# Performance work log

Hardware: AMD Instinct MI355X
Metric: run time of the kernel (lower is better)

Reference implementation:

```python
import jax, jax.numpy as jnp
import numpy as np

N = 100000   # nodes
E = 1600000  # edges (before self-loops)
H = 4        # heads
C = 16       # out channels per head
NEG_SLOPE = 0.2


def _gat_layer(x, src, dst, W, a_src, a_dst, b):
    # x: [N, Fin]; W: [Fin, H*C]; a_src/a_dst: [H, C]; b: [H*C]
    h = (x @ W).reshape(N, H, C)                       # [N, H, C]
    e_s = jnp.einsum('nhc,hc->nh', h, a_src)           # [N, H]
    e_d = jnp.einsum('nhc,hc->nh', h, a_dst)           # [N, H]
    e = e_s[src] + e_d[dst]                            # [E', H]
    e = jax.nn.leaky_relu(e, NEG_SLOPE)
    # segment softmax over destination nodes
    m = jax.ops.segment_max(e, dst, num_segments=N)    # [N, H]
    ex = jnp.exp(e - m[dst])
    s = jax.ops.segment_sum(ex, dst, num_segments=N)   # [N, H]
    alpha = ex / (s[dst] + 1e-16)                      # [E', H]
    msg = alpha[:, :, None] * h[src]                   # [E', H, C]
    out = jax.ops.segment_sum(msg, dst, num_segments=N)  # [N, H, C]
    return out.reshape(N, H * C) + b


def setup_inputs() -> dict:
    key = jax.random.key(0)
    ks = jax.random.split(key, 24)
    g = lambda k, shp, sc=0.1: (jax.random.normal(k, shp, jnp.float32) * sc)
    inp = {
        'x': jax.random.normal(ks[0], (N, 1), jnp.float32),
        'edge_index': jax.random.randint(ks[1], (2, E), 0, N, dtype=jnp.int32),
        # GAT layer 0: in=1
        'W0': g(ks[2], (1, H * C)), 'as0': g(ks[3], (H, C)), 'ad0': g(ks[4], (H, C)), 'b0': jnp.zeros((H * C,), jnp.float32),
        # GAT layer 1: in=64
        'W1': g(ks[5], (H * C, H * C)), 'as1': g(ks[6], (H, C)), 'ad1': g(ks[7], (H, C)), 'b1': jnp.zeros((H * C,), jnp.float32),
        # GAT layer 2: in=64
        'W2': g(ks[8], (H * C, H * C)), 'as2': g(ks[9], (H, C)), 'ad2': g(ks[10], (H, C)), 'b2': jnp.zeros((H * C,), jnp.float32),
        # latent MLP: Linear(64,64) -> ReLU -> Linear(64,16)
        'lw1': g(ks[11], (H * C, 64)), 'lb1': jnp.zeros((64,), jnp.float32),
        'lw2': g(ks[12], (64, 16)), 'lb2': jnp.zeros((16,), jnp.float32),
        # decoder: Linear(16,4) -> Softmax
        'dw': g(ks[13], (16, 4)), 'db': jnp.zeros((4,), jnp.float32),
    }
    return inp


def reference(x, edge_index, W0, as0, ad0, b0, W1, as1, ad1, b1, W2, as2, ad2, b2, lw1, lb1, lw2, lb2, dw, db):
    # add self-loops (PyG GATConv default add_self_loops=True)
    loops = jnp.arange(N, dtype=edge_index.dtype)
    src = jnp.concatenate([edge_index[0], loops])
    dst = jnp.concatenate([edge_index[1], loops])
    h = _gat_layer(x, src, dst, W0, as0, ad0, b0)
    h = _gat_layer(h, src, dst, W1, as1, ad1, b1)
    h = _gat_layer(h, src, dst, W2, as2, ad2, b2)
    h = jax.nn.relu(h @ lw1 + lb1)
    h = h @ lw2 + lb2
    logits = h @ dw + db
    return jax.nn.softmax(logits, axis=-1)
```

## Files before the change

kernel.cpp:

```cpp
#include <hip/hip_runtime.h>
#include <hip/hip_fp16.h>
#include <math.h>

#define NN 100000
#define EE 1600000
#define EP (EE + NN)
#define NEG 0.2f
#define TN 128
#define BW 256
#define NB 391
#define CHUNK 4096
#define SSTRIDE 5120
#define SCAP 5120

typedef __attribute__((ext_vector_type(2))) float floatx2;

__device__ inline unsigned pk_fp8x4(float a, float b, float c, float d) {
    unsigned r = __builtin_amdgcn_cvt_pk_fp8_f32(a, b, 0u, false);
    r = __builtin_amdgcn_cvt_pk_fp8_f32(c, d, r, true);
    return r;
}

__device__ __forceinline__ void accum_fp8p(uint2 raw, float p, floatx2* acc) {
    floatx2 p2; p2[0] = p; p2[1] = p;
    acc[0] += p2 * __builtin_amdgcn_cvt_pk_f32_fp8(raw.x, false);
    acc[1] += p2 * __builtin_amdgcn_cvt_pk_f32_fp8(raw.x, true);
    acc[2] += p2 * __builtin_amdgcn_cvt_pk_f32_fp8(raw.y, false);
    acc[3] += p2 * __builtin_amdgcn_cvt_pk_f32_fp8(raw.y, true);
}

__device__ __forceinline__ int wave_iscan(int v, int lane) {
#pragma unroll
    for (int o = 1; o < 64; o <<= 1) {
        int t = __shfl_up(v, o);
        if (lane >= o) v += t;
    }
    return v;
}


__global__ __launch_bounds__(512) void partition_k(const int* __restrict__ ei, int* __restrict__ gcur,
                                                   unsigned int* __restrict__ arena) {
    __shared__ int lh[512], lcur[512], lbase[512];
    __shared__ int wsum[8];
    __shared__ unsigned int staged[CHUNK];
    __shared__ unsigned short stb[CHUNK];
    int tid = threadIdx.x;
    int lane = tid & 63, wid = tid >> 6;
    int c0 = blockIdx.x * CHUNK;
    int csize = min(CHUNK, EP - c0);
    lh[tid] = 0;
    __syncthreads();
    unsigned int myv[8];
    int myb[8];
#pragma unroll
    for (int i = 0; i < 8; i++) {
        int e = c0 + i * 512 + tid;
        if (e < c0 + csize) {
            int d = (e < EE) ? ei[EE + e] : (e - EE);
            int sv = (e < EE) ? ei[e] : d;
            int b = d >> 8;
            myv[i] = ((unsigned)(d - (b << 8)) << 17) | (unsigned)sv;
            myb[i] = b;
            atomicAdd(&lh[b], 1);
        } else myb[i] = -1;
    }
    __syncthreads();
    int v = lh[tid];
    int isc = wave_iscan(v, lane);
    if (lane == 63) wsum[wid] = isc;
    __syncthreads();
    if (tid == 0) {
        int run = 0;
#pragma unroll
        for (int w = 0; w < 8; w++) { int t = wsum[w]; wsum[w] = run; run += t; }
    }
    __syncthreads();
    int excl = isc - v + wsum[wid];
    lcur[tid] = excl;
    __syncthreads();
#pragma unroll
    for (int i = 0; i < 8; i++) {
        if (myb[i] >= 0) {
            int idx = atomicAdd(&lcur[myb[i]], 1);
            staged[idx] = myv[i];
            stb[idx] = (unsigned short)myb[i];
        }
    }
    __syncthreads();
    if (tid < NB && v > 0) {
        int base = atomicAdd(&gcur[tid], v);
        lbase[tid] = tid * SSTRIDE + base - excl;
    }
    __syncthreads();
    for (int i = tid; i < csize; i += 512) {
        unsigned int val = staged[i];
        arena[lbase[stb[i]] + i] = val;
    }
}

__global__ __launch_bounds__(512) void bscan_k(const int* __restrict__ gcur, int* __restrict__ bbase,
                                               int* __restrict__ rowptr) {
    __shared__ int s[512];
    int tid = threadIdx.x;
    int v = (tid < NB) ? gcur[tid] : 0;
    s[tid] = v;
    __syncthreads();
    for (int o = 1; o < 512; o <<= 1) {
        int t = (tid >= o) ? s[tid - o] : 0;
        __syncthreads();
        s[tid] += t;
        __syncthreads();
    }
    int excl = s[tid] - v;
    if (tid <= NB) bbase[tid] = excl;
    if (tid == 0) rowptr[NN] = EP;
}

__global__ __launch_bounds__(512) void csr_scatter_k(const int* __restrict__ bbase, const int* __restrict__ gcur,
                                                     const unsigned int* __restrict__ arena,
                                                     int* __restrict__ rowptr, int* __restrict__ edge_src) {
    __shared__ int cnt[256], sc[256];
    __shared__ int wsum[4];
    __shared__ unsigned int stg[SCAP];
    int tid = threadIdx.x;
    int b = blockIdx.x;
    int e0 = bbase[b];
    int sz = gcur[b];
    int abase = b * SSTRIDE;
    if (tid < 256) cnt[tid] = 0;
    __syncthreads();
    for (int i = tid; i < sz; i += 512) {
        unsigned int v = arena[abase + i];
        if (i < SCAP) stg[i] = v;
        atomicAdd(&cnt[v >> 17], 1);
    }
    __syncthreads();
    if (tid < 256) {
        int lane = tid & 63, wid = tid >> 6;
        int v = cnt[tid];
        int isc = wave_iscan(v, lane);
        if (lane == 63) wsum[wid] = isc;
        __syncthreads();
        if (tid == 0) {
            int run = 0;
#pragma unroll
            for (int w = 0; w < 4; w++) { int t = wsum[w]; wsum[w] = run; run += t; }
        }
        __syncthreads();
        int excl = isc - v + wsum[wid];
        int d = (b << 8) + tid;
        if (d < NN) rowptr[d] = e0 + excl;
        sc[tid] = excl;
    } else {
        __syncthreads();
        __syncthreads();
    }
    __syncthreads();
    for (int i = tid; i < sz; i += 512) {
        unsigned int val = (i < SCAP) ? stg[i] : arena[abase + i];
        int dl = val >> 17;
        int p = atomicAdd(&sc[dl], 1);
        edge_src[e0 + p] = (int)(val & 0x1FFFFu);
    }
}


__global__ __launch_bounds__(256) void gather0_k(const float* __restrict__ x, const float* __restrict__ W0,
                                                 const float* __restrict__ as_, const float* __restrict__ ad_,
                                                 const int* __restrict__ rowptr, const int* __restrict__ edge_src,
                                                 const float* __restrict__ b, __half* __restrict__ hout) {
    __shared__ float W0l[64], asl[64], adl[64], bl[64];
    int tid = threadIdx.x;
    if (tid < 64) { W0l[tid] = W0[tid]; asl[tid] = as_[tid]; adl[tid] = ad_[tid]; bl[tid] = b[tid]; }
    __syncthreads();
    int wv = (blockIdx.x * 256 + tid) >> 6;
    int lane = tid & 63;
    if (wv >= NN) return;
    int q = lane >> 2, head = lane & 3;
    float cs = 0.f, cd = 0.f;
#pragma unroll
    for (int c = 0; c < 16; c++) {
        float w = W0l[head * 16 + c];
        cs += w * asl[head * 16 + c];
        cd += w * adl[head * 16 + c];
    }
    int beg = rowptr[wv], end = rowptr[wv + 1];
    float xd = x[wv];
    float num = 0.f, den = 0.f;
    for (int e0 = beg; e0 < end; e0 += 16) {
        int e = e0 + q;
        bool vld = e < end;
        int ee = vld ? e : (end - 1);
        int src = edge_src[ee];
        float xs = x[src];
        float ev = xs * cs + xd * cd;
        ev = ev > 0.f ? ev : NEG * ev;
        float p = vld ? __expf(ev) : 0.f;
        num += p * xs;
        den += p;
    }
    num += __shfl_xor(num, 4);  num += __shfl_xor(num, 8);
    num += __shfl_xor(num, 16); num += __shfl_xor(num, 32);
    den += __shfl_xor(den, 4);  den += __shfl_xor(den, 8);
    den += __shfl_xor(den, 16); den += __shfl_xor(den, 32);
    float nh = __shfl(num, lane >> 4);
    float dh = __shfl(den, lane >> 4);
    float val = nh / (dh + 1e-16f);
    float hv = val * W0l[lane] + bl[lane];
    hout[((size_t)wv << 6) + lane] = __float2half(hv);
}


__global__ __launch_bounds__(256) void transform64_k(const __half* __restrict__ hin, const float* __restrict__ W,
                                                     const float* __restrict__ as_, const float* __restrict__ ad_,
                                                     unsigned char* __restrict__ h8, float* __restrict__ es, float* __restrict__ ed) {
    __shared__ float At[64 * TN];
    __shared__ float Wl[64 * 64];
    int tid = threadIdx.x;
    for (int i = tid; i < 4096; i += 256) Wl[i] = W[i];
    int n0 = blockIdx.x * TN;
    {
        int row = tid >> 1, hf = tid & 1;
        int n = n0 + row;
        const uint4* src = (const uint4*)(hin + ((size_t)n << 6) + (hf << 5));
#pragma unroll
        for (int i = 0; i < 4; i++) {
            uint4 raw = make_uint4(0, 0, 0, 0);
            if (n < NN) raw = src[i];
            __half2* hh = (__half2*)&raw;
            int c = (hf << 5) + (i << 3);
#pragma unroll
            for (int j = 0; j < 4; j++) {
                float2 f = __half22float2(hh[j]);
                At[(c + 2 * j) * TN + row]     = f.x;
                At[(c + 2 * j + 1) * TN + row] = f.y;
            }
        }
    }
    __syncthreads();
    int c = tid & 15, r = tid >> 4;
    float acc[8][4];
#pragma unroll
    for (int i = 0; i < 8; i++)
#pragma unroll
        for (int j = 0; j < 4; j++) acc[i][j] = 0.f;
#pragma unroll 4
    for (int k = 0; k < 64; k++) {
        float4 a0 = *(float4*)&At[k * TN + r * 8];
        float4 a1 = *(float4*)&At[k * TN + r * 8 + 4];
        float4 w  = *(float4*)&Wl[k * 64 + c * 4];
        float av[8] = {a0.x, a0.y, a0.z, a0.w, a1.x, a1.y, a1.z, a1.w};
#pragma unroll
        for (int i = 0; i < 8; i++) {
            acc[i][0] += av[i] * w.x; acc[i][1] += av[i] * w.y;
            acc[i][2] += av[i] * w.z; acc[i][3] += av[i] * w.w;
        }
    }
    int head = c >> 2, qq = c & 3;
    float as0v = as_[head * 16 + qq * 4], as1v = as_[head * 16 + qq * 4 + 1];
    float as2v = as_[head * 16 + qq * 4 + 2], as3v = as_[head * 16 + qq * 4 + 3];
    float ad0v = ad_[head * 16 + qq * 4], ad1v = ad_[head * 16 + qq * 4 + 1];
    float ad2v = ad_[head * 16 + qq * 4 + 2], ad3v = ad_[head * 16 + qq * 4 + 3];
#pragma unroll
    for (int i = 0; i < 8; i++) {
        int n = n0 + r * 8 + i;
        float pes = acc[i][0] * as0v + acc[i][1] * as1v + acc[i][2] * as2v + acc[i][3] * as3v;
        float ped = acc[i][0] * ad0v + acc[i][1] * ad1v + acc[i][2] * ad2v + acc[i][3] * ad3v;
        pes += __shfl_xor(pes, 1); pes += __shfl_xor(pes, 2);
        ped += __shfl_xor(ped, 1); ped += __shfl_xor(ped, 2);
        if (n < NN) {
            unsigned rq = pk_fp8x4(acc[i][0], acc[i][1], acc[i][2], acc[i][3]);
            *(unsigned*)(h8 + ((size_t)n << 6) + (c << 2)) = rq;
            if (qq == 0) { es[n * 4 + head] = pes; ed[n * 4 + head] = ped; }
        }
    }
}


__global__ __launch_bounds__(256) void gather_k(const unsigned char* __restrict__ h8, const float* __restrict__ es,
                                                const float* __restrict__ ed, const int* __restrict__ rowptr,
                                                const int* __restrict__ edge_src, const float* __restrict__ b,
                                                __half* __restrict__ hout) {
    int pr = (blockIdx.x * 256 + threadIdx.x) >> 6;
    int lane = threadIdx.x & 63;
    int nA = pr * 2;
    if (nA >= NN) return;
    int nB = nA + 1;
    bool hasB = nB < NN;
    int q = lane >> 3, j = lane & 7, head = j >> 1;
    const unsigned char* h8j = h8 + (j << 3);
    int begA = rowptr[nA], endA = rowptr[nA + 1];
    int begB = hasB ? rowptr[nB] : begA, endB = hasB ? rowptr[nB + 1] : begA;
    float edvA = ed[nA * 4 + head];
    float edvB = hasB ? ed[nB * 4 + head] : 0.f;
    floatx2 accA[4], accB[4];
#pragma unroll
    for (int t = 0; t < 4; t++) { accA[t] = (floatx2)(0.f); accB[t] = (floatx2)(0.f); }
    float sA = 0.f, sB = 0.f;
    int iters = max((endA - begA + 7) >> 3, (endB - begB + 7) >> 3);
    for (int k = 0; k < iters; k++) {
        int eA = begA + (k << 3) + q;
        int eB = begB + (k << 3) + q;
        bool vA = eA < endA;
        bool vB = eB < endB;
        int srcA = edge_src[vA ? eA : begA];
        int srcB = edge_src[vB ? eB : begB];
        uint2 rawA = *(const uint2*)(h8j + ((unsigned)srcA << 6));
        float esvA = es[srcA * 4 + head];
        uint2 rawB = *(const uint2*)(h8j + ((unsigned)srcB << 6));
        float esvB = es[srcB * 4 + head];
        float evA = esvA + edvA; evA = evA > 0.f ? evA : NEG * evA;
        float evB = esvB + edvB; evB = evB > 0.f ? evB : NEG * evB;
        float pA = vA ? __expf(evA) : 0.f;
        float pB = vB ? __expf(evB) : 0.f;
        accum_fp8p(rawA, pA, accA);
        accum_fp8p(rawB, pB, accB);
        sA += pA;
        sB += pB;
    }
    float fA[8], fB[8];
#pragma unroll
    for (int t = 0; t < 4; t++) {
        fA[2 * t] = accA[t][0]; fA[2 * t + 1] = accA[t][1];
        fB[2 * t] = accB[t][0]; fB[2 * t + 1] = accB[t][1];
    }
#pragma unroll
    for (int t = 0; t < 8; t++) {
        fA[t] += __shfl_xor(fA[t], 8);
        fA[t] += __shfl_xor(fA[t], 16);
        fA[t] += __shfl_xor(fA[t], 32);
        fB[t] += __shfl_xor(fB[t], 8);
        fB[t] += __shfl_xor(fB[t], 16);
        fB[t] += __shfl_xor(fB[t], 32);
    }
    sA += __shfl_xor(sA, 8); sA += __shfl_xor(sA, 16); sA += __shfl_xor(sA, 32);
    sB += __shfl_xor(sB, 8); sB += __shfl_xor(sB, 16); sB += __shfl_xor(sB, 32);
    if (q == 0) {
        const float4* bp = (const float4*)(b + j * 8);
        float4 b0 = bp[0], b1 = bp[1];
        {
            float inv = 1.0f / (sA + 1e-16f);
            union { __half2 h2[4]; uint4 u; } pk;
            pk.h2[0] = __floats2half2_rn(fA[0] * inv + b0.x, fA[1] * inv + b0.y);
            pk.h2[1] = __floats2half2_rn(fA[2] * inv + b0.z, fA[3] * inv + b0.w);
            pk.h2[2] = __floats2half2_rn(fA[4] * inv + b1.x, fA[5] * inv + b1.y);
            pk.h2[3] = __floats2half2_rn(fA[6] * inv + b1.z, fA[7] * inv + b1.w);
            *(uint4*)(hout + ((size_t)nA << 6) + (j << 3)) = pk.u;
        }
        if (hasB) {
            float inv = 1.0f / (sB + 1e-16f);
            union { __half2 h2[4]; uint4 u; } pk;
            pk.h2[0] = __floats2half2_rn(fB[0] * inv + b0.x, fB[1] * inv + b0.y);
            pk.h2[1] = __floats2half2_rn(fB[2] * inv + b0.z, fB[3] * inv + b0.w);
            pk.h2[2] = __floats2half2_rn(fB[4] * inv + b1.x, fB[5] * inv + b1.y);
            pk.h2[3] = __floats2half2_rn(fB[6] * inv + b1.z, fB[7] * inv + b1.w);
            *(uint4*)(hout + ((size_t)nB << 6) + (j << 3)) = pk.u;
        }
    }
}


__global__ __launch_bounds__(256) void mlp_k(const __half* __restrict__ h, const float* __restrict__ lw1,
                                             const float* __restrict__ lb1, const float* __restrict__ lw2,
                                             const float* __restrict__ lb2, const float* __restrict__ dw,
                                             const float* __restrict__ db, float* __restrict__ out) {
    __shared__ float At[64 * TN];
    __shared__ float W1l[4096];
    __shared__ float W2l[1024];
    __shared__ float dwl[64];
    __shared__ float dbl[4];
    int tid = threadIdx.x;
    for (int i = tid; i < 4096; i += 256) W1l[i] = lw1[i];
    for (int i = tid; i < 1024; i += 256) W2l[i] = lw2[i];
    if (tid < 64) dwl[tid] = dw[tid];
    if (tid < 4) dbl[tid] = db[tid];
    int n0 = blockIdx.x * TN;
    {
        int row = tid >> 1, hf = tid & 1;
        int n = n0 + row;
        const uint4* src = (const uint4*)(h + ((size_t)n << 6) + (hf << 5));
#pragma unroll
        for (int i = 0; i < 4; i++) {
            uint4 raw = make_uint4(0, 0, 0, 0);
            if (n < NN) raw = src[i];
            __half2* hh = (__half2*)&raw;
            int c = (hf << 5) + (i << 3);
#pragma unroll
            for (int j = 0; j < 4; j++) {
                float2 f = __half22float2(hh[j]);
                At[(c + 2 * j) * TN + row]     = f.x;
                At[(c + 2 * j + 1) * TN + row] = f.y;
            }
        }
    }
    __syncthreads();
    int c = tid & 15, r = tid >> 4;
    float acc[8][4];
#pragma unroll
    for (int i = 0; i < 8; i++)
#pragma unroll
        for (int j = 0; j < 4; j++) acc[i][j] = 0.f;
#pragma unroll 4
    for (int k = 0; k < 64; k++) {
        float4 a0 = *(float4*)&At[k * TN + r * 8];
        float4 a1 = *(float4*)&At[k * TN + r * 8 + 4];
        float4 w  = *(float4*)&W1l[k * 64 + c * 4];
        float av[8] = {a0.x, a0.y, a0.z, a0.w, a1.x, a1.y, a1.z, a1.w};
#pragma unroll
        for (int i = 0; i < 8; i++) {
            acc[i][0] += av[i] * w.x; acc[i][1] += av[i] * w.y;
            acc[i][2] += av[i] * w.z; acc[i][3] += av[i] * w.w;
        }
    }
    float b1v0 = lb1[c * 4], b1v1 = lb1[c * 4 + 1], b1v2 = lb1[c * 4 + 2], b1v3 = lb1[c * 4 + 3];
    __syncthreads();
#pragma unroll
    for (int i = 0; i < 8; i++) {
        int n = r * 8 + i;
        At[(c * 4 + 0) * TN + n] = fmaxf(acc[i][0] + b1v0, 0.f);
        At[(c * 4 + 1) * TN + n] = fmaxf(acc[i][1] + b1v1, 0.f);
        At[(c * 4 + 2) * TN + n] = fmaxf(acc[i][2] + b1v2, 0.f);
        At[(c * 4 + 3) * TN + n] = fmaxf(acc[i][3] + b1v3, 0.f);
    }
    __syncthreads();
    float acc2[8];
#pragma unroll
    for (int i = 0; i < 8; i++) acc2[i] = 0.f;
#pragma unroll 4
    for (int k = 0; k < 64; k++) {
        float4 a0 = *(float4*)&At[k * TN + r * 8];
        float4 a1 = *(float4*)&At[k * TN + r * 8 + 4];
        float wv = W2l[k * 16 + c];
        acc2[0] += a0.x * wv; acc2[1] += a0.y * wv; acc2[2] += a0.z * wv; acc2[3] += a0.w * wv;
        acc2[4] += a1.x * wv; acc2[5] += a1.y * wv; acc2[6] += a1.z * wv; acc2[7] += a1.w * wv;
    }
    float b2v = lb2[c];
#pragma unroll
    for (int i = 0; i < 8; i++) W1l[c * TN + r * 8 + i] = acc2[i] + b2v;
    __syncthreads();
    if (tid < TN) {
        int n = n0 + tid;
        if (n < NN) {
            float lg0 = dbl[0], lg1 = dbl[1], lg2 = dbl[2], lg3 = dbl[3];
#pragma unroll
            for (int k = 0; k < 16; k++) {
                float a = W1l[k * TN + tid];
                lg0 += a * dwl[k * 4];     lg1 += a * dwl[k * 4 + 1];
                lg2 += a * dwl[k * 4 + 2]; lg3 += a * dwl[k * 4 + 3];
            }
            float mx = fmaxf(fmaxf(lg0, lg1), fmaxf(lg2, lg3));
            float e0 = __expf(lg0 - mx), e1 = __expf(lg1 - mx), e2 = __expf(lg2 - mx), e3 = __expf(lg3 - mx);
            float inv = 1.0f / (e0 + e1 + e2 + e3);
            *(float4*)(out + (size_t)n * 4) = make_float4(e0 * inv, e1 * inv, e2 * inv, e3 * inv);
        }
    }
}


extern "C" void kernel_launch(void* const* d_in, const int* in_sizes, int n_in,
                              void* d_out, int out_size, void* d_ws, size_t ws_size,
                              hipStream_t stream) {
    const float* x   = (const float*)d_in[0];
    const int*   ei  = (const int*)d_in[1];
    const float* W0  = (const float*)d_in[2];
    const float* as0 = (const float*)d_in[3];
    const float* ad0 = (const float*)d_in[4];
    const float* b0  = (const float*)d_in[5];
    const float* W1  = (const float*)d_in[6];
    const float* as1 = (const float*)d_in[7];
    const float* ad1 = (const float*)d_in[8];
    const float* b1  = (const float*)d_in[9];
    const float* W2  = (const float*)d_in[10];
    const float* as2 = (const float*)d_in[11];
    const float* ad2 = (const float*)d_in[12];
    const float* b2  = (const float*)d_in[13];
    const float* lw1 = (const float*)d_in[14];
    const float* lb1 = (const float*)d_in[15];
    const float* lw2 = (const float*)d_in[16];
    const float* lb2 = (const float*)d_in[17];
    const float* dw  = (const float*)d_in[18];
    const float* db  = (const float*)d_in[19];
    float* out = (float*)d_out;

    char* p = (char*)d_ws;
    size_t off = 0;
    auto alloc = [&](size_t n) -> void* {
        void* r = p + off;
        off = (off + n + 255) & ~(size_t)255;
        return r;
    };
    __half* hB     = (__half*)alloc((size_t)NN * 64 * 2);
    __half* hC     = (__half*)alloc((size_t)NN * 64 * 2);
    unsigned char* h8 = (unsigned char*)alloc((size_t)NN * 64);
    float*  es     = (float*)alloc((size_t)NN * 4 * 4);
    float*  ed     = (float*)alloc((size_t)NN * 4 * 4);
    int*    rowptr = (int*)alloc((size_t)(NN + 1) * 4);
    int*    edge_src = (int*)alloc((size_t)EP * 4);
    unsigned int* arena = (unsigned int*)alloc((size_t)NB * SSTRIDE * 4);
    int*    gcur   = (int*)alloc(512 * 4);
    int*    bbase  = (int*)alloc(513 * 4);

    hipMemsetAsync(gcur, 0, 512 * 4, stream);

    partition_k<<<(EP + CHUNK - 1) / CHUNK, 512, 0, stream>>>(ei, gcur, arena);
    bscan_k<<<1, 512, 0, stream>>>(gcur, bbase, rowptr);
    csr_scatter_k<<<NB, 512, 0, stream>>>(bbase, gcur, arena, rowptr, edge_src);

    int nb_tile = (NN + TN - 1) / TN;
    int nb_wave = (NN + 3) / 4;
    int nb_pair = ((NN + 1) / 2 + 3) / 4;

    gather0_k<<<nb_wave, 256, 0, stream>>>(x, W0, as0, ad0, rowptr, edge_src, b0, hB);

    transform64_k<<<nb_tile, 256, 0, stream>>>(hB, W1, as1, ad1, h8, es, ed);
    gather_k<<<nb_pair, 256, 0, stream>>>(h8, es, ed, rowptr, edge_src, b1, hC);

    transform64_k<<<nb_tile, 256, 0, stream>>>(hC, W2, as2, ad2, h8, es, ed);
    gather_k<<<nb_pair, 256, 0, stream>>>(h8, es, ed, rowptr, edge_src, b2, hB);

    mlp_k<<<nb_tile, 256, 0, stream>>>(hB, lw1, lb1, lw2, lb2, dw, db, out);
}
```

Measured before the change: 309.8 us.

## Sort nodes by degree for balanced gather and fold bucket scan into partition

```diff
diff --git a/kernel.cpp b/kernel.cpp
--- a/kernel.cpp
+++ b/kernel.cpp
@@ -40,7 +40,8 @@
 
 
 __global__ __launch_bounds__(512) void partition_k(const int* __restrict__ ei, int* __restrict__ gcur,
-                                                   unsigned int* __restrict__ arena) {
+                                                   unsigned int* __restrict__ arena,
+                                                   int* __restrict__ bbase, int* __restrict__ rowptr) {
     __shared__ int lh[512], lcur[512], lbase[512];
     __shared__ int wsum[8];
     __shared__ unsigned int staged[CHUNK];
@@ -97,29 +98,34 @@
         unsigned int val = staged[i];
         arena[lbase[stb[i]] + i] = val;
     }
-}
-
-__global__ __launch_bounds__(512) void bscan_k(const int* __restrict__ gcur, int* __restrict__ bbase,
-                                               int* __restrict__ rowptr) {
-    __shared__ int s[512];
-    int tid = threadIdx.x;
-    int v = (tid < NB) ? gcur[tid] : 0;
-    s[tid] = v;
-    __syncthreads();
-    for (int o = 1; o < 512; o <<= 1) {
-        int t = (tid >= o) ? s[tid - o] : 0;
-        __syncthreads();
-        s[tid] += t;
-        __syncthreads();
-    }
-    int excl = s[tid] - v;
-    if (tid <= NB) bbase[tid] = excl;
-    if (tid == 0) rowptr[NN] = EP;
+    __threadfence();
+    __syncthreads();
+    if (tid == 0) {
+        unsigned prev = atomicAdd((unsigned int*)&gcur[500], 1u);
+        lh[0] = (prev == (unsigned)(gridDim.x - 1)) ? 1 : 0;
+    }
+    __syncthreads();
+    if (lh[0]) {
+        __threadfence();
+        int v2 = (tid < NB) ? gcur[tid] : 0;
+        lcur[tid] = v2;
+        __syncthreads();
+        for (int o = 1; o < 512; o <<= 1) {
+            int t = (tid >= o) ? lcur[tid - o] : 0;
+            __syncthreads();
+            lcur[tid] += t;
+            __syncthreads();
+        }
+        int ex2 = lcur[tid] - v2;
+        if (tid <= NB) bbase[tid] = ex2;
+        if (tid == 0) rowptr[NN] = EP;
+    }
 }
 
 __global__ __launch_bounds__(512) void csr_scatter_k(const int* __restrict__ bbase, const int* __restrict__ gcur,
                                                      const unsigned int* __restrict__ arena,
-                                                     int* __restrict__ rowptr, int* __restrict__ edge_src) {
+                                                     int* __restrict__ rowptr, int* __restrict__ edge_src,
+                                                     int* __restrict__ dbin) {
     __shared__ int cnt[256], sc[256];
     __shared__ int wsum[4];
     __shared__ unsigned int stg[SCAP];
@@ -150,7 +156,10 @@
         __syncthreads();
         int excl = isc - v + wsum[wid];
         int d = (b << 8) + tid;
-        if (d < NN) rowptr[d] = e0 + excl;
+        if (d < NN) {
+            rowptr[d] = e0 + excl;
+            atomicAdd(&dbin[v > 255 ? 255 : v], 1);
+        }
         sc[tid] = excl;
     } else {
         __syncthreads();
@@ -165,18 +174,45 @@
     }
 }
 
+__global__ __launch_bounds__(256) void dscan_k(const int* __restrict__ dbin, int* __restrict__ dcur) {
+    __shared__ int s[256];
+    int tid = threadIdx.x;
+    int v = dbin[tid];
+    s[tid] = v;
+    __syncthreads();
+    for (int o = 1; o < 256; o <<= 1) {
+        int t = (tid >= o) ? s[tid - o] : 0;
+        __syncthreads();
+        s[tid] += t;
+        __syncthreads();
+    }
+    dcur[tid] = s[tid] - v;
+}
+
+__global__ __launch_bounds__(256) void dscatter_k(const int* __restrict__ rowptr, int* __restrict__ dcur,
+                                                  int* __restrict__ porder) {
+    int n = blockIdx.x * 256 + threadIdx.x;
+    if (n >= NN) return;
+    int deg = rowptr[n + 1] - rowptr[n];
+    int bin = deg > 255 ? 255 : deg;
+    int idx = atomicAdd(&dcur[bin], 1);
+    porder[idx] = n;
+}
+
 
 __global__ __launch_bounds__(256) void gather0_k(const float* __restrict__ x, const float* __restrict__ W0,
                                                  const float* __restrict__ as_, const float* __restrict__ ad_,
                                                  const int* __restrict__ rowptr, const int* __restrict__ edge_src,
+                                                 const int* __restrict__ porder,
                                                  const float* __restrict__ b, __half* __restrict__ hout) {
     __shared__ float W0l[64], asl[64], adl[64], bl[64];
     int tid = threadIdx.x;
     if (tid < 64) { W0l[tid] = W0[tid]; asl[tid] = as_[tid]; adl[tid] = ad_[tid]; bl[tid] = b[tid]; }
     __syncthreads();
-    int wv = (blockIdx.x * 256 + tid) >> 6;
+    int pr = (blockIdx.x * 256 + tid) >> 6;
     int lane = tid & 63;
-    if (wv >= NN) return;
+    if (pr >= NN) return;
+    int wv = porder[pr];
     int q = lane >> 2, head = lane & 3;
     float cs = 0.f, cd = 0.f;
 #pragma unroll
@@ -280,20 +316,19 @@
 
 __global__ __launch_bounds__(256) void gather_k(const unsigned char* __restrict__ h8, const float* __restrict__ es,
                                                 const float* __restrict__ ed, const int* __restrict__ rowptr,
-                                                const int* __restrict__ edge_src, const float* __restrict__ b,
-                                                __half* __restrict__ hout) {
+                                                const int* __restrict__ edge_src, const int* __restrict__ porder,
+                                                const float* __restrict__ b, __half* __restrict__ hout) {
     int pr = (blockIdx.x * 256 + threadIdx.x) >> 6;
     int lane = threadIdx.x & 63;
-    int nA = pr * 2;
-    if (nA >= NN) return;
-    int nB = nA + 1;
-    bool hasB = nB < NN;
+    if (pr * 2 >= NN) return;
+    int nA = porder[pr * 2];
+    int nB = (pr * 2 + 1 < NN) ? porder[pr * 2 + 1] : nA;
     int q = lane >> 3, j = lane & 7, head = j >> 1;
     const unsigned char* h8j = h8 + (j << 3);
     int begA = rowptr[nA], endA = rowptr[nA + 1];
-    int begB = hasB ? rowptr[nB] : begA, endB = hasB ? rowptr[nB + 1] : begA;
+    int begB = rowptr[nB], endB = rowptr[nB + 1];
     float edvA = ed[nA * 4 + head];
-    float edvB = hasB ? ed[nB * 4 + head] : 0.f;
+    float edvB = ed[nB * 4 + head];
     floatx2 accA[4], accB[4];
 #pragma unroll
     for (int t = 0; t < 4; t++) { accA[t] = (floatx2)(0.f); accB[t] = (floatx2)(0.f); }
@@ -348,7 +383,7 @@
             pk.h2[3] = __floats2half2_rn(fA[6] * inv + b1.z, fA[7] * inv + b1.w);
             *(uint4*)(hout + ((size_t)nA << 6) + (j << 3)) = pk.u;
         }
-        if (hasB) {
+        if (nB != nA) {
             float inv = 1.0f / (sB + 1e-16f);
             union { __half2 h2[4]; uint4 u; } pk;
             pk.h2[0] = __floats2half2_rn(fB[0] * inv + b0.x, fB[1] * inv + b0.y);
@@ -497,27 +532,32 @@
     float*  ed     = (float*)alloc((size_t)NN * 4 * 4);
     int*    rowptr = (int*)alloc((size_t)(NN + 1) * 4);
     int*    edge_src = (int*)alloc((size_t)EP * 4);
+    int*    porder = (int*)alloc((size_t)NN * 4);
     unsigned int* arena = (unsigned int*)alloc((size_t)NB * SSTRIDE * 4);
-    int*    gcur   = (int*)alloc(512 * 4);
+    int*    ints   = (int*)alloc(1024 * 4);
     int*    bbase  = (int*)alloc(513 * 4);
-
-    hipMemsetAsync(gcur, 0, 512 * 4, stream);
-
-    partition_k<<<(EP + CHUNK - 1) / CHUNK, 512, 0, stream>>>(ei, gcur, arena);
-    bscan_k<<<1, 512, 0, stream>>>(gcur, bbase, rowptr);
-    csr_scatter_k<<<NB, 512, 0, stream>>>(bbase, gcur, arena, rowptr, edge_src);
+    int* gcur = ints;
+    int* dbin = ints + 512;
+    int* dcur = ints + 768;
+
+    hipMemsetAsync(ints, 0, 1024 * 4, stream);
+
+    partition_k<<<(EP + CHUNK - 1) / CHUNK, 512, 0, stream>>>(ei, gcur, arena, bbase, rowptr);
+    csr_scatter_k<<<NB, 512, 0, stream>>>(bbase, gcur, arena, rowptr, edge_src, dbin);
+    dscan_k<<<1, 256, 0, stream>>>(dbin, dcur);
+    dscatter_k<<<(NN + 255) / 256, 256, 0, stream>>>(rowptr, dcur, porder);
 
     int nb_tile = (NN + TN - 1) / TN;
     int nb_wave = (NN + 3) / 4;
     int nb_pair = ((NN + 1) / 2 + 3) / 4;
 
-    gather0_k<<<nb_wave, 256, 0, stream>>>(x, W0, as0, ad0, rowptr, edge_src, b0, hB);
+    gather0_k<<<nb_wave, 256, 0, stream>>>(x, W0, as0, ad0, rowptr, edge_src, porder, b0, hB);
 
     transform64_k<<<nb_tile, 256, 0, stream>>>(hB, W1, as1, ad1, h8, es, ed);
-    gather_k<<<nb_pair, 256, 0, stream>>>(h8, es, ed, rowptr, edge_src, b1, hC);
+    gather_k<<<nb_pair, 256, 0, stream>>>(h8, es, ed, rowptr, edge_src, porder, b1, hC);
 
     transform64_k<<<nb_tile, 256, 0, stream>>>(hC, W2, as2, ad2, h8, es, ed);
-    gather_k<<<nb_pair, 256, 0, stream>>>(h8, es, ed, rowptr, edge_src, b2, hB);
+    gather_k<<<nb_pair, 256, 0, stream>>>(h8, es, ed, rowptr, edge_src, porder, b2, hB);
 
     mlp_k<<<nb_tile, 256, 0, stream>>>(hB, lw1, lb1, lw2, lb2, dw, db, out);
 }
```

Measured after the change: 961.3 us. 210% more time.
